# Kernel tuning notes

Measured on AMD Instinct MI355X. Metric: run time of the kernel, lower is better.

Reference implementation:

```python
import jax, jax.numpy as jnp
import numpy as np

B, C, H, W, NMAX = 16, 1, 128, 8192, 64


def setup_inputs() -> dict:
    key = jax.random.key(0)
    x = jax.random.normal(key, (B, C, H, W), dtype=jnp.float32)
    # Build realistic non-overlapping, sorted chirp boundaries with numpy.
    rng = np.random.default_rng(0)
    slot = W // NMAX  # 128 columns per chirp slot
    gaps = rng.integers(0, 40, size=(B, NMAX))
    widths = rng.integers(20, slot - 40, size=(B, NMAX))
    starts = np.arange(NMAX)[None, :] * slot + gaps
    ends = starts + widths
    n = rng.integers(48, NMAX + 1, size=(B,)).astype(np.int32)
    xi = np.stack([starts, ends], axis=-1).astype(np.int32)
    valid = np.arange(NMAX)[None, :] < n[:, None]
    xi = xi * valid[:, :, None]  # zero out invalid rows
    return {
        "x": x,
        "xi": jnp.asarray(xi),
        "N": jnp.asarray(n),
        "sep_param": jnp.zeros((1, 1, 1), dtype=jnp.float32),  # learned sep token scalar
    }


def reference(x, xi, N, sep_param):
    """Vectorized TinyBird.compactify_data: remove silence between chirp
    blocks, packing blocks contiguously with 1-column separators.
    Returns (x_new, xi_new). x_new keeps full width W (original truncates
    to data-dependent w_max; padding beyond w_max is zeros, same values)."""
    Bb, Cc, Hh, Ww = x.shape
    nmax = xi.shape[1]
    idx = jnp.arange(nmax, dtype=jnp.int32)[None, :]            # (1, Nmax)
    Nc = N.reshape(Bb, 1).astype(jnp.int32)                      # (B, 1)
    w = jnp.clip(xi[:, :, 1] - xi[:, :, 0], 0, None).astype(jnp.int32)
    valid = idx < Nc                                             # (B, Nmax)
    wv = jnp.where(valid, w, 0)
    csum = jnp.cumsum(wv, axis=1)
    start_new = csum - wv + idx                                  # compressed starts
    end_new = csum + idx                                         # compressed ends
    xi_new = jnp.where(valid[:, :, None],
                       jnp.stack([start_new, end_new], axis=-1), 0).astype(xi.dtype)

    # For every output column j, find which compressed segment it falls in.
    j = jnp.arange(Ww, dtype=jnp.int32)
    big = jnp.int32(Ww + nmax + 2)
    start_search = jnp.where(valid, start_new, big)              # keep sorted
    seg = jax.vmap(lambda s: jnp.searchsorted(s, j, side='right'))(start_search) - 1
    seg = jnp.clip(seg, 0, nmax - 1)                             # (B, W)
    bidx = jnp.arange(Bb)[:, None]
    s_new = start_new[bidx, seg]
    e_new = end_new[bidx, seg]
    seg_valid = valid[bidx, seg]
    in_seg = seg_valid & (j[None, :] >= s_new) & (j[None, :] < e_new)
    is_sep = seg_valid & (j[None, :] == e_new) & (seg < (Nc - 1))
    src = jnp.clip(xi[bidx, seg, 0].astype(jnp.int32) + (j[None, :] - s_new), 0, Ww - 1)
    src_full = jnp.broadcast_to(src[:, None, None, :], (Bb, Cc, Hh, Ww))
    gathered = jnp.take_along_axis(x, src_full, axis=3)          # ragged gather
    sep_val = sep_param[0, 0, 0]                                 # sep_token column value
    x_new = jnp.where(in_seg[:, None, None, :], gathered,
                      jnp.where(is_sep[:, None, None, :], sep_val, jnp.float32(0)))
    return x_new, xi_new
```

## Files before the change

### kernel.cpp

```cpp
#include <hip/hip_runtime.h>

#define Bn 16
#define Hn 128
#define Wn 8192
#define NMAX 64

#define SEG_BLKS 64
#define ZERO_BLKS 32
#define BLKS_PER_B (SEG_BLKS + ZERO_BLKS)
#define ROWS_PER_ZB (Hn / ZERO_BLKS)

typedef float nt_f4 __attribute__((ext_vector_type(4)));

__global__ __launch_bounds__(256) void pack_rect_kernel(
    const float* __restrict__ x, const int* __restrict__ xi,
    const int* __restrict__ N, const float* __restrict__ sep_param,
    float* __restrict__ out, float* __restrict__ out_xi) {
    const int b    = blockIdx.y;
    const int k    = blockIdx.x;
    const int tid  = threadIdx.x;
    const int lane = tid & 63;
    const int wave = tid >> 6;

    const int nb = N[b];
    const int s0 = xi[(b * NMAX + lane) * 2 + 0];
    const int s1 = xi[(b * NMAX + lane) * 2 + 1];
    int w = s1 - s0; if (w < 0) w = 0;
    const bool valid = lane < nb;
    const int wv = valid ? w : 0;
    int c = wv;
    #pragma unroll
    for (int d = 1; d < 64; d <<= 1) {
        int t = __shfl_up(c, d, 64);
        if (lane >= d) c += t;
    }
    const int start_new = c - wv + lane;
    const int end_new   = c + lane;

    if (k == 0 && wave == 0) {
        out_xi[(b * NMAX + lane) * 2 + 0] = valid ? (float)start_new : 0.0f;
        out_xi[(b * NMAX + lane) * 2 + 1] = valid ? (float)end_new   : 0.0f;
    }

    const float sep = sep_param[0];
    float* __restrict__ ob = out + (size_t)b * Hn * Wn;

    if (k < SEG_BLKS) {
        const int seg = k;
        if (seg >= nb) return;
        const int seg_s = __shfl(start_new, seg);
        const int seg_w = __shfl(wv, seg);
        const int seg_a = __shfl(s0, seg);
        const int wtot  = seg_w + ((seg < nb - 1) ? 1 : 0);
        const float* __restrict__ xb = x + (size_t)b * Hn * Wn;

        for (int c0 = 0; c0 < wtot; c0 += 64) {
            const int col = c0 + lane;
            if (col < wtot) {
                const bool is_data = col < seg_w;
                const int  src     = seg_a + col;
                const int  dst     = seg_s + col;
                for (int rr = 0; rr < 32; rr += 8) {
                    float v[8];
                    #pragma unroll
                    for (int i = 0; i < 8; ++i) {
                        const int r = wave + 4 * (rr + i);
                        v[i] = is_data ? xb[(size_t)r * Wn + src] : sep;
                    }
                    #pragma unroll
                    for (int i = 0; i < 8; ++i) {
                        const int r = wave + 4 * (rr + i);
                        __builtin_nontemporal_store(v[i], &ob[(size_t)r * Wn + dst]);
                    }
                }
            }
        }
    } else {
        const int tail = (nb > 0) ? __shfl(end_new, nb - 1) : 0;
        const int t4   = (tail + 3) & ~3;
        const int r0   = (k - SEG_BLKS) * ROWS_PER_ZB;
        const nt_f4 z4 = {0.0f, 0.0f, 0.0f, 0.0f};
        for (int r = r0; r < r0 + ROWS_PER_ZB; ++r) {
            float* __restrict__ orow = ob + (size_t)r * Wn;
            if (tid < (t4 - tail))
                __builtin_nontemporal_store(0.0f, &orow[tail + tid]);
            nt_f4* orow4 = reinterpret_cast<nt_f4*>(orow);
            for (int i4 = (t4 >> 2) + tid; i4 < (Wn >> 2); i4 += 256) {
                __builtin_nontemporal_store(z4, &orow4[i4]);
            }
        }
    }
}

extern "C" void kernel_launch(void* const* d_in, const int* in_sizes, int n_in,
                              void* d_out, int out_size, void* d_ws, size_t ws_size,
                              hipStream_t stream) {
    const float* x   = (const float*)d_in[0];
    const int* xi    = (const int*)d_in[1];
    const int* N     = (const int*)d_in[2];
    const float* sep = (const float*)d_in[3];

    float* out_x  = (float*)d_out;
    float* out_xi = (float*)d_out + (size_t)Bn * Hn * Wn;

    dim3 grid(BLKS_PER_B, Bn);
    pack_rect_kernel<<<grid, 256, 0, stream>>>(x, xi, N, sep, out_x, out_xi);
}
```

Before: 132.5 us.

## Switch from per-segment scatter to output-tiled gather with per-column binary search

Instead of one block per segment scattering columns plus separate zero-fill blocks, each block now owns a 256-column by 32-row output tile. Every thread binary-searches the compressed segment starts through wave shuffles to find its source column, then gathers and writes float4 nontemporal stores. This is meant to balance work evenly across blocks and vectorise every output write, replacing the scalar stores and uneven per-segment loads. The cost is that every block repeats the prefix scan and a 6-step search per column, and the reads become scalar gathers that may be misaligned.

```diff
diff --git a/kernel.cpp b/kernel.cpp
--- a/kernel.cpp
+++ b/kernel.cpp
@@ -5,19 +5,21 @@
 #define Wn 8192
 #define NMAX 64
 
-#define SEG_BLKS 64
-#define ZERO_BLKS 32
-#define BLKS_PER_B (SEG_BLKS + ZERO_BLKS)
-#define ROWS_PER_ZB (Hn / ZERO_BLKS)
+#define TILE 256
+#define RPB 32
+#define CT (Wn / TILE)
+#define RB (Hn / RPB)
 
 typedef float nt_f4 __attribute__((ext_vector_type(4)));
 
-__global__ __launch_bounds__(256) void pack_rect_kernel(
+__global__ __launch_bounds__(256) void pack_tile_kernel(
     const float* __restrict__ x, const int* __restrict__ xi,
     const int* __restrict__ N, const float* __restrict__ sep_param,
     float* __restrict__ out, float* __restrict__ out_xi) {
     const int b    = blockIdx.y;
-    const int k    = blockIdx.x;
+    const int tb   = blockIdx.x;
+    const int tile = tb & (CT - 1);
+    const int rblk = tb >> 5;
     const int tid  = threadIdx.x;
     const int lane = tid & 63;
     const int wave = tid >> 6;
@@ -26,8 +28,7 @@
     const int s0 = xi[(b * NMAX + lane) * 2 + 0];
     const int s1 = xi[(b * NMAX + lane) * 2 + 1];
     int w = s1 - s0; if (w < 0) w = 0;
-    const bool valid = lane < nb;
-    const int wv = valid ? w : 0;
+    const int wv = (lane < nb) ? w : 0;
     int c = wv;
     #pragma unroll
     for (int d = 1; d < 64; d <<= 1) {
@@ -37,58 +38,55 @@
     const int start_new = c - wv + lane;
     const int end_new   = c + lane;
 
-    if (k == 0 && wave == 0) {
+    if (tb == 0 && wave == 0) {
+        const bool valid = lane < nb;
         out_xi[(b * NMAX + lane) * 2 + 0] = valid ? (float)start_new : 0.0f;
         out_xi[(b * NMAX + lane) * 2 + 1] = valid ? (float)end_new   : 0.0f;
     }
 
     const float sep = sep_param[0];
-    float* __restrict__ ob = out + (size_t)b * Hn * Wn;
 
-    if (k < SEG_BLKS) {
-        const int seg = k;
-        if (seg >= nb) return;
-        const int seg_s = __shfl(start_new, seg);
-        const int seg_w = __shfl(wv, seg);
-        const int seg_a = __shfl(s0, seg);
-        const int wtot  = seg_w + ((seg < nb - 1) ? 1 : 0);
-        const float* __restrict__ xb = x + (size_t)b * Hn * Wn;
+    const int cbase = tile * TILE + lane * 4;
+    int  srcc[4];
+    float fillv[4];
+    bool isdat[4];
+    #pragma unroll
+    for (int q = 0; q < 4; ++q) {
+        const int j = cbase + q;
+        int lo = 0;
+        #pragma unroll
+        for (int s = 32; s >= 1; s >>= 1) {
+            const int mid = lo + s;
+            const int sm = __shfl(start_new, mid & 63);
+            if (mid < NMAX && sm <= j) lo = mid;
+        }
+        const int st  = __shfl(start_new, lo);
+        const int wd  = __shfl(wv, lo);
+        const int sc  = __shfl(s0, lo);
+        const int off = j - st;
+        isdat[q] = off < wd;
+        const bool issep = (off == wd) && (lo < nb - 1);
+        srcc[q]  = sc + off;
+        fillv[q] = issep ? sep : 0.0f;
+    }
 
-        for (int c0 = 0; c0 < wtot; c0 += 64) {
-            const int col = c0 + lane;
-            if (col < wtot) {
-                const bool is_data = col < seg_w;
-                const int  src     = seg_a + col;
-                const int  dst     = seg_s + col;
-                for (int rr = 0; rr < 32; rr += 8) {
-                    float v[8];
-                    #pragma unroll
-                    for (int i = 0; i < 8; ++i) {
-                        const int r = wave + 4 * (rr + i);
-                        v[i] = is_data ? xb[(size_t)r * Wn + src] : sep;
-                    }
-                    #pragma unroll
-                    for (int i = 0; i < 8; ++i) {
-                        const int r = wave + 4 * (rr + i);
-                        __builtin_nontemporal_store(v[i], &ob[(size_t)r * Wn + dst]);
-                    }
-                }
-            }
-        }
-    } else {
-        const int tail = (nb > 0) ? __shfl(end_new, nb - 1) : 0;
-        const int t4   = (tail + 3) & ~3;
-        const int r0   = (k - SEG_BLKS) * ROWS_PER_ZB;
-        const nt_f4 z4 = {0.0f, 0.0f, 0.0f, 0.0f};
-        for (int r = r0; r < r0 + ROWS_PER_ZB; ++r) {
-            float* __restrict__ orow = ob + (size_t)r * Wn;
-            if (tid < (t4 - tail))
-                __builtin_nontemporal_store(0.0f, &orow[tail + tid]);
-            nt_f4* orow4 = reinterpret_cast<nt_f4*>(orow);
-            for (int i4 = (t4 >> 2) + tid; i4 < (Wn >> 2); i4 += 256) {
-                __builtin_nontemporal_store(z4, &orow4[i4]);
-            }
-        }
+    const int rbase = rblk * RPB + wave * 8;
+    const float* __restrict__ xb = x + (size_t)b * Hn * Wn;
+    float* __restrict__ ob = out + (size_t)b * Hn * Wn + cbase;
+
+    float4 v[8];
+    #pragma unroll
+    for (int i = 0; i < 8; ++i) {
+        const float* __restrict__ rp = xb + (size_t)(rbase + i) * Wn;
+        v[i].x = isdat[0] ? rp[srcc[0]] : fillv[0];
+        v[i].y = isdat[1] ? rp[srcc[1]] : fillv[1];
+        v[i].z = isdat[2] ? rp[srcc[2]] : fillv[2];
+        v[i].w = isdat[3] ? rp[srcc[3]] : fillv[3];
+    }
+    #pragma unroll
+    for (int i = 0; i < 8; ++i) {
+        nt_f4 t = {v[i].x, v[i].y, v[i].z, v[i].w};
+        __builtin_nontemporal_store(t, (nt_f4*)(ob + (size_t)(rbase + i) * Wn));
     }
 }
 
@@ -103,6 +101,6 @@
     float* out_x  = (float*)d_out;
     float* out_xi = (float*)d_out + (size_t)Bn * Hn * Wn;
 
-    dim3 grid(BLKS_PER_B, Bn);
-    pack_rect_kernel<<<grid, 256, 0, stream>>>(x, xi, N, sep, out_x, out_xi);
+    dim3 grid(CT * RB, Bn);
+    pack_tile_kernel<<<grid, 256, 0, stream>>>(x, xi, N, sep, out_x, out_xi);
 }
```

Measured after the change: 127.5 us. 3.8% less time.
